# Kernel optimization log

Hardware: AMD Instinct MI355X
Metric: run time of the kernel (lower is better)

The kernel has to match this reference:

```python
import jax, jax.numpy as jnp
import numpy as np
import math

B, T, N, C = 1, 12, 10000, 32
TIME_DIM, N_SUP, E, NODE_EMB = 8, 3, 320000, 32
S = N_SUP + 2  # support_len + 2 slots after concat


def setup_inputs() -> dict:
    key = jax.random.key(0)
    ks = jax.random.split(key, 16)
    inp = {
        'x': jax.random.normal(ks[0], (B, T, N, C), jnp.float32),
        'timeoh': jax.random.uniform(ks[1], (B, 43), jnp.float32),
        'edges': jax.random.randint(ks[2], (N_SUP, 2, E), 0, N),
        # shared dy_gat params (attention_list reuses the same ModuleList)
        'mlp_w': jax.random.normal(ks[3], (C, C), jnp.float32) * 0.05,
        'mlp_b': jnp.zeros((C,), jnp.float32),
        'temb_w': jax.random.normal(ks[4], (43, TIME_DIM), jnp.float32) * 0.1,
        'atten_pool': jax.random.normal(ks[5], (TIME_DIM, 2 * C), jnp.float32) * 0.1,
        # adaptive-adjacency gcn branch
        'node2vec': jax.random.normal(ks[6], (N, NODE_EMB), jnp.float32) * 0.1,
        'gcn_w': jax.random.normal(ks[7], (3 * C, C), jnp.float32) * 0.05,
        'gcn_b': jnp.zeros((C,), jnp.float32),
        # slot self-attention over S supports
        'q_w': jax.random.normal(ks[8], (C, 6 * C), jnp.float32) * 0.05,
        'q_b': jnp.zeros((6 * C,), jnp.float32),
        'k_w': jax.random.normal(ks[9], (C, 6 * C), jnp.float32) * 0.05,
        'k_b': jnp.zeros((6 * C,), jnp.float32),
        'v_w': jax.random.normal(ks[10], (C, 6 * C), jnp.float32) * 0.05,
        'v_b': jnp.zeros((6 * C,), jnp.float32),
        'dense_w': jax.random.normal(ks[11], (6 * C, C), jnp.float32) * 0.05,
        'dense_b': jnp.zeros((C,), jnp.float32),
    }
    return inp


def _dy_gat(x, timeoh, src, dst, mlp_w, mlp_b, temb_w, atten_pool):
    h = x @ mlp_w + mlp_b                                   # (B,T,N,C)
    attn = (timeoh @ temb_w) @ atten_pool                    # (B,2C)
    # einsum('btnc,bc->btn') over concatenated [h_src, h_dst] splits additively
    s_src = jnp.einsum('btnc,bc->btn', h, attn[:, :C])
    s_dst = jnp.einsum('btnc,bc->btn', h, attn[:, C:])
    values = s_src[:, :, src] + s_dst[:, :, dst]             # (B,T,E)
    p = jax.nn.leaky_relu(values, 0.01)
    e = jnp.exp(p - jnp.max(p, axis=2, keepdims=True))       # global (per b,t) max-shift
    rowsum = jnp.zeros((B, T, N), e.dtype).at[:, :, src].add(e)
    h_prime = jnp.zeros_like(h).at[:, :, src].add(e[..., None] * h[:, :, dst, :])
    h_prime = h_prime / (rowsum[..., None] + 9e-15)
    return jax.nn.elu(h_prime)  # concat=True


def reference(x, timeoh, edges, mlp_w, mlp_b, temb_w, atten_pool,
              node2vec, gcn_w, gcn_b, q_w, q_b, k_w, k_b, v_w, v_b,
              dense_w, dense_b):
    outs = [x]
    for i in range(N_SUP):
        outs.append(_dy_gat(x, timeoh, edges[i, 0], edges[i, 1],
                            mlp_w, mlp_b, temb_w, atten_pool))
    # adaptive graph conv (static, order=2, support_len=1)
    adj = jax.nn.softmax(jax.nn.relu(node2vec @ node2vec.T), axis=1)  # (N,N)
    x1 = jnp.einsum('wv,btvf->btwf', adj, x)
    x2 = jnp.einsum('wv,btvf->btwf', adj, x1)
    x_adp = jnp.concatenate([x, x1, x2], -1) @ gcn_w + gcn_b
    outs.append(x_adp)
    out = jnp.concatenate(outs, -1).reshape(B, T, N, S, C)
    q = out @ q_w + q_b                                       # (B,T,N,S,6C)
    k = out @ k_w + k_b
    v = out @ v_w + v_b
    scores = jnp.einsum('btnsd,btnud->btnsu', q, k) / math.sqrt(6 * C)
    a = jax.nn.softmax(scores, axis=-1)
    o = jnp.einsum('btnsu,btnud->btnsd', a, v)
    o = o @ dense_w + dense_b                                 # (B,T,N,S,C)
    return jax.nn.elu(jnp.mean(o, axis=-2))                   # (B,T,N,C)
```

## Files before the change

kernel.cpp:

```cpp
#include <hip/hip_runtime.h>
#include <hip/hip_bf16.h>

#define T_ 12
#define N_ 10000
#define C_ 32
#define E_ 320000
#define SUP_ 3
#define TN_ (T_*N_)

typedef __attribute__((ext_vector_type(4))) float f32x4;
typedef __attribute__((ext_vector_type(8))) short bf16x8;
typedef __attribute__((ext_vector_type(4))) short bf16x4;

__device__ __forceinline__ short bf16c(float f) {
  __hip_bfloat16 b = __float2bfloat16(f);
  return (short)__builtin_bit_cast(unsigned short, b);
}

#if __has_builtin(__builtin_amdgcn_exp2f)
#define EXP2F(x) __builtin_amdgcn_exp2f(x)
#else
#define EXP2F(x) exp2f(x)
#endif

#define PRM_ATTN 0
#define PRM_G    64
#define PRM_H    1088
#define PRM_G1   2112
#define PRM_G2   2144
#define PRM_HB   2176
#define PRM_G0   2208

__global__ __launch_bounds__(256) void k_prep(
    const float* __restrict__ timeoh, const float* __restrict__ temb_w,
    const float* __restrict__ atten_pool,
    const float* __restrict__ q_w, const float* __restrict__ q_b,
    const float* __restrict__ k_w, const float* __restrict__ k_b,
    const float* __restrict__ v_w, const float* __restrict__ v_b,
    const float* __restrict__ dense_w, const float* __restrict__ dense_b,
    float* __restrict__ prm) {
  __shared__ float tv[8];
  int tid = threadIdx.x;
  if (tid < 8) {
    float s = 0.f;
    for (int j = 0; j < 43; j++) s += timeoh[j] * temb_w[j * 8 + tid];
    tv[tid] = s;
  }
  __syncthreads();
  if (tid < 64) {
    float s = 0.f;
    for (int d = 0; d < 8; d++) s += tv[d] * atten_pool[d * 64 + tid];
    prm[PRM_ATTN + tid] = s;
  }
  for (int idx = tid; idx < 1024; idx += 256) {
    int r = idx >> 5, c = idx & 31;
    float s = 0.f, s2 = 0.f;
    for (int d = 0; d < 192; d++) {
      s  += q_w[r * 192 + d] * k_w[c * 192 + d];
      s2 += v_w[r * 192 + d] * dense_w[d * 32 + c];
    }
    prm[PRM_G + idx] = s;
    prm[PRM_H + idx] = s2;
  }
  if (tid < 32) {
    float s = 0.f, s2 = 0.f, s3 = 0.f;
    for (int d = 0; d < 192; d++) {
      s  += q_w[tid * 192 + d] * k_b[d];
      s2 += k_w[tid * 192 + d] * q_b[d];
      s3 += v_b[d] * dense_w[d * 32 + tid];
    }
    prm[PRM_G1 + tid] = s;
    prm[PRM_G2 + tid] = s2;
    prm[PRM_HB + tid] = s3 + dense_b[tid];
  }
  if (tid == 0) {
    float s = 0.f;
    for (int d = 0; d < 192; d++) s += q_b[d] * k_b[d];
    prm[PRM_G0] = s;
  }
}

__global__ __launch_bounds__(256) void k_h(
    const float* __restrict__ x, const float* __restrict__ mlp_w,
    const float* __restrict__ mlp_b, const float* __restrict__ prm,
    __hip_bfloat16* __restrict__ h16, float* __restrict__ s_src,
    float* __restrict__ s_dst) {
  __shared__ float W[32 * 32];
  __shared__ float bsh[32], attnsh[64];
  __shared__ float xs[8][32];
  int tid = threadIdx.x;
  for (int i = tid; i < 1024; i += 256) W[i] = mlp_w[i];
  if (tid < 32) bsh[tid] = mlp_b[tid];
  if (tid < 64) attnsh[tid] = prm[PRM_ATTN + tid];
  long base = (long)blockIdx.x * 8;
  int nloc = tid >> 5, c = tid & 31;
  long row = base + nloc;
  xs[nloc][c] = x[row * 32 + c];
  __syncthreads();
  float hval = bsh[c];
#pragma unroll
  for (int k = 0; k < 32; k++) hval = fmaf(xs[nloc][k], W[k * 32 + c], hval);
  h16[row * 32 + c] = __float2bfloat16(hval);
  float a = hval * attnsh[c], b = hval * attnsh[32 + c];
#pragma unroll
  for (int m = 16; m >= 1; m >>= 1) {
    a += __shfl_xor(a, m, 64);
    b += __shfl_xor(b, m, 64);
  }
  if (c == 0) { s_src[row] = a; s_dst[row] = b; }
}

__global__ __launch_bounds__(256) void k_maxs(const float* __restrict__ ssrc,
                                              const float* __restrict__ sdst,
                                              float* __restrict__ Mt) {
  __shared__ float sh[8];
  const int t = blockIdx.x, tid = threadIdx.x;
  float ma = -1e30f, mb = -1e30f;
  for (int i = tid; i < N_; i += 256) {
    ma = fmaxf(ma, ssrc[(long)t * N_ + i]);
    mb = fmaxf(mb, sdst[(long)t * N_ + i]);
  }
#pragma unroll
  for (int k = 32; k >= 1; k >>= 1) {
    ma = fmaxf(ma, __shfl_xor(ma, k, 64));
    mb = fmaxf(mb, __shfl_xor(mb, k, 64));
  }
  if ((tid & 63) == 0) { sh[(tid >> 6) * 2] = ma; sh[(tid >> 6) * 2 + 1] = mb; }
  __syncthreads();
  if (tid == 0) {
    float A = fmaxf(fmaxf(sh[0], sh[2]), fmaxf(sh[4], sh[6]));
    float B = fmaxf(fmaxf(sh[1], sh[3]), fmaxf(sh[5], sh[7]));
    Mt[t] = A + B;
  }
}

__global__ __launch_bounds__(256) void k_hist(const int* __restrict__ edges,
                                              int* __restrict__ cnt) {
  int sup = blockIdx.y;
  int e = blockIdx.x * 256 + threadIdx.x;
  const int* src = edges + (long)sup * 2 * E_;
  atomicAdd(&cnt[sup * N_ + src[e]], 1);
}

__global__ __launch_bounds__(1024) void k_scan(const int* __restrict__ cnt,
                                               int* __restrict__ offs,
                                               int* __restrict__ cur) {
  __shared__ int sh[1024];
  __shared__ int run;
  int sup = blockIdx.x, tid = threadIdx.x;
  if (tid == 0) run = 0;
  __syncthreads();
  for (int base = 0; base < N_; base += 1024) {
    int i = base + tid;
    int v = (i < N_) ? cnt[sup * N_ + i] : 0;
    sh[tid] = v;
    __syncthreads();
    for (int off = 1; off < 1024; off <<= 1) {
      int t = (tid >= off) ? sh[tid - off] : 0;
      __syncthreads();
      sh[tid] += t;
      __syncthreads();
    }
    int runv = run;
    int excl = runv + sh[tid] - v;
    if (i < N_) {
      offs[sup * (N_ + 1) + i] = excl;
      cur[sup * N_ + i] = excl;
    }
    __syncthreads();
    if (tid == 0) run = runv + sh[1023];
    __syncthreads();
  }
  if (tid == 0) offs[sup * (N_ + 1) + N_] = run;
}

__global__ __launch_bounds__(256) void k_fill(const int* __restrict__ edges,
                                              int* __restrict__ cur,
                                              int* __restrict__ csr) {
  int sup = blockIdx.y;
  int e = blockIdx.x * 256 + threadIdx.x;
  const int* src = edges + (long)sup * 2 * E_;
  const int* dst = src + E_;
  int pos = atomicAdd(&cur[sup * N_ + src[e]], 1);
  csr[sup * E_ + pos] = dst[e];
}

__global__ __launch_bounds__(256) void k_gather(
    const int* __restrict__ csr, const int* __restrict__ offs,
    const float* __restrict__ s_src, const float* __restrict__ s_dst,
    const float* __restrict__ Mt, const __hip_bfloat16* __restrict__ h16,
    __hip_bfloat16* __restrict__ hp16) {
  const int sup = blockIdx.z, t = blockIdx.y;
  const int wave = threadIdx.x >> 6, lane = threadIdx.x & 63;
  const int n = blockIdx.x * 4 + wave;
  const float M = Mt[t];
  const float a = s_src[(long)t * N_ + n];
  const int off = offs[sup * (N_ + 1) + n], end = offs[sup * (N_ + 1) + n + 1];
  const float* sd = s_dst + (long)t * N_;
  const uint4* hb4 = (const uint4*)(h16 + (long)t * N_ * 32);
  const int* csrs = csr + sup * E_;
  const int slot = lane >> 2, cl = lane & 3;
  const int clamp = (end > off) ? (end - 1) : 0;

  float acc[8];
#pragma unroll
  for (int j = 0; j < 8; j++) acc[j] = 0.f;
  float psum = 0.f;

  const int idx0 = off + slot;
  int d0 = csrs[min(idx0, clamp)];
  int d1 = csrs[min(idx0 + 16, clamp)];
  float sd0 = sd[d0];
  uint4 u0 = hb4[d0 * 4 + cl];

  for (int idx = idx0; idx < end; idx += 16) {
    int d2 = csrs[min(idx + 32, clamp)];
    float sd1 = sd[d1];
    uint4 u1 = hb4[d1 * 4 + cl];
    float v = a + sd0;
    v = fmaxf(v, 0.01f * v);
    float p = __expf(v - M);
    psum += p;
    acc[0] = fmaf(p, __uint_as_float(u0.x << 16),        acc[0]);
    acc[1] = fmaf(p, __uint_as_float(u0.x & 0xffff0000u), acc[1]);
    acc[2] = fmaf(p, __uint_as_float(u0.y << 16),        acc[2]);
    acc[3] = fmaf(p, __uint_as_float(u0.y & 0xffff0000u), acc[3]);
    acc[4] = fmaf(p, __uint_as_float(u0.z << 16),        acc[4]);
    acc[5] = fmaf(p, __uint_as_float(u0.z & 0xffff0000u), acc[5]);
    acc[6] = fmaf(p, __uint_as_float(u0.w << 16),        acc[6]);
    acc[7] = fmaf(p, __uint_as_float(u0.w & 0xffff0000u), acc[7]);
    d1 = d2; sd0 = sd1; u0 = u1;
  }

#pragma unroll
  for (int m = 4; m <= 32; m <<= 1) psum += __shfl_xor(psum, m, 64);
#pragma unroll
  for (int j = 0; j < 8; j++) {
#pragma unroll
    for (int m = 4; m <= 32; m <<= 1) acc[j] += __shfl_xor(acc[j], m, 64);
  }

  if (slot == 0) {
    float inv = 1.f / (psum + 9e-15f);
    unsigned w[4];
#pragma unroll
    for (int q = 0; q < 4; q++) {
      float h0 = acc[2 * q + 0] * inv;
      float h1 = acc[2 * q + 1] * inv;
      h0 = (h0 > 0.f) ? h0 : (__expf(h0) - 1.f);
      h1 = (h1 > 0.f) ? h1 : (__expf(h1) - 1.f);
      unsigned lo = (unsigned)(unsigned short)__builtin_bit_cast(unsigned short, __float2bfloat16(h0));
      unsigned hi = (unsigned)(unsigned short)__builtin_bit_cast(unsigned short, __float2bfloat16(h1));
      w[q] = lo | (hi << 16);
    }
    ((uint4*)hp16)[((long)sup * TN_ + (long)t * N_ + n) * 4 + cl] = uint4{w[0], w[1], w[2], w[3]};
  }
}

__global__ __launch_bounds__(256) void k_n2vA(const float* __restrict__ n2v,
                                              short* __restrict__ n2vA) {
  const float SC = 1.2011224087864498f;
  int idx = blockIdx.x * 256 + threadIdx.x;
  if (idx >= N_ * 4) return;
  int row = idx >> 2, l4 = idx & 3;
  short v[8];
#pragma unroll
  for (int h = 0; h < 2; h++)
#pragma unroll
    for (int j = 0; j < 4; j++)
      v[h * 4 + j] = bf16c(n2v[row * 32 + 16 * h + 4 * l4 + j] * SC);
  *(bf16x8*)&n2vA[(long)idx * 8] = bf16x8{v[0], v[1], v[2], v[3], v[4], v[5], v[6], v[7]};
}

template <int WITHR>
__global__ __launch_bounds__(256) void k_pack(const float* __restrict__ src,
                                              const float* __restrict__ rinv,
                                              short* __restrict__ xq) {
  int idx = blockIdx.x * 256 + threadIdx.x;
  int ck = idx / 1536;
  int rem = idx - ck * 1536;
  int l4 = rem / 384;
  int col = rem - l4 * 384;
  int t = col >> 5, f = col & 31;
  const long cb = (long)t * N_ * 32 + f;
  short v[8];
#pragma unroll
  for (int e = 0; e < 8; e++) {
    int vv = ck * 32 + 4 * l4 + (e & 3) + 16 * (e >> 2);
    float a = 0.f;
    if (vv < N_) {
      a = src[cb + (long)vv * 32];
      if (WITHR) a *= rinv[vv];
    }
    v[e] = bf16c(a);
  }
  *(bf16x8*)&xq[(long)idx * 8] = bf16x8{v[0], v[1], v[2], v[3], v[4], v[5], v[6], v[7]};
}

template <int PASS>
__global__ __launch_bounds__(512, 2) void k_adj12(const short* __restrict__ n2vA,
                                                  const short* __restrict__ xq,
                                                  float* __restrict__ out,
                                                  float* __restrict__ Rout) {
  __shared__ __align__(16) short aPl[2][8 * 4 * 64 * 8];
  const int tid = threadIdx.x;
  const int lane = tid & 63;
  const int wv = tid >> 6;
  const int l15 = lane & 15;
  const int l4 = lane >> 4;
  const int brow0 = blockIdx.x * 64;
  const int colbase = wv * 48;

  bf16x8 bw[4];
#pragma unroll
  for (int mt = 0; mt < 4; mt++) {
    int row = brow0 + mt * 16 + l15;
    row = row < N_ ? row : N_ - 1;
    bw[mt] = *(const bf16x8*)&n2vA[((long)row * 4 + l4) * 8];
  }

  f32x4 acc[4][3];
#pragma unroll
  for (int i = 0; i < 4; i++)
#pragma unroll
    for (int j = 0; j < 3; j++) acc[i][j] = f32x4{0.f, 0.f, 0.f, 0.f};
  float racc[4] = {0.f, 0.f, 0.f, 0.f};

#define PHASE_A(cexpr, slab)                                                              \
  {                                                                                       \
    const int c_ = (cexpr);                                                               \
    if (c_ < 313) {                                                                       \
      const int vb_ = c_ * 32;                                                            \
      int r1_ = vb_ + 16 + l15; r1_ = r1_ < N_ ? r1_ : N_ - 1;                            \
      bf16x8 av0_ = *(const bf16x8*)&n2vA[((long)(vb_ + l15) * 4 + l4) * 8];              \
      bf16x8 av1_ = *(const bf16x8*)&n2vA[((long)r1_ * 4 + l4) * 8];                      \
      _Pragma("unroll")                                                                   \
      for (int mt = 0; mt < 4; mt++) {                                                    \
        f32x4 s0_ = __builtin_amdgcn_mfma_f32_16x16x32_bf16(av0_, bw[mt],                 \
                                                            f32x4{0.f,0.f,0.f,0.f},0,0,0);\
        f32x4 s1_ = __builtin_amdgcn_mfma_f32_16x16x32_bf16(av1_, bw[mt],                 \
                                                            f32x4{0.f,0.f,0.f,0.f},0,0,0);\
        short pp_[8];                                                                     \
        float rs0_ = 0.f, rs1_ = 0.f;                                                     \
        _Pragma("unroll")                                                                 \
        for (int j = 0; j < 4; j++) {                                                     \
          float p0_ = EXP2F(fmaxf(s0_[j], 0.f));                                          \
          float p1_ = EXP2F(fmaxf(s1_[j], 0.f));                                          \
          if constexpr (PASS == 1) { rs0_ += p0_; rs1_ += p1_; }                          \
          pp_[j] = bf16c(p0_);                                                            \
          pp_[j + 4] = bf16c(p1_);                                                        \
        }                                                                                 \
        *(bf16x8*)&aPl[slab][((wv * 4 + mt) * 64 + lane) * 8] =                           \
            bf16x8{pp_[0],pp_[1],pp_[2],pp_[3],pp_[4],pp_[5],pp_[6],pp_[7]};              \
        if constexpr (PASS == 1) racc[mt] += (c_ != 312) ? (rs0_ + rs1_) : rs0_;          \
      }                                                                                   \
    }                                                                                     \
  }

  PHASE_A(wv, 0)
  __syncthreads();

  for (int g = 0; g < 40; g++) {
    const int cur = g & 1;
    if (g + 1 < 40) PHASE_A((g + 1) * 8 + wv, cur ^ 1)

    const int rem = 313 - g * 8;
    if (rem >= 8) {
      bf16x8 bx[24];
#pragma unroll
      for (int cc = 0; cc < 8; cc++) {
        const long xb = (long)(g * 8 + cc) * 1536 + (long)l4 * 384;
        bx[cc * 3 + 0] = *(const bf16x8*)&xq[(xb + colbase + 0 * 16 + l15) * 8];
        bx[cc * 3 + 1] = *(const bf16x8*)&xq[(xb + colbase + 1 * 16 + l15) * 8];
        bx[cc * 3 + 2] = *(const bf16x8*)&xq[(xb + colbase + 2 * 16 + l15) * 8];
      }
#pragma unroll
      for (int cc = 0; cc < 8; cc++) {
#pragma unroll
        for (int mt = 0; mt < 4; mt++) {
          bf16x8 aP = *(const bf16x8*)&aPl[cur][((cc * 4 + mt) * 64 + lane) * 8];
          acc[mt][0] = __builtin_amdgcn_mfma_f32_16x16x32_bf16(aP, bx[cc * 3 + 0], acc[mt][0], 0, 0, 0);
          acc[mt][1] = __builtin_amdgcn_mfma_f32_16x16x32_bf16(aP, bx[cc * 3 + 1], acc[mt][1], 0, 0, 0);
          acc[mt][2] = __builtin_amdgcn_mfma_f32_16x16x32_bf16(aP, bx[cc * 3 + 2], acc[mt][2], 0, 0, 0);
        }
      }
    } else {
      for (int cc = 0; cc < rem; cc++) {
        const long xb = (long)(g * 8 + cc) * 1536 + (long)l4 * 384;
        bf16x8 bx0 = *(const bf16x8*)&xq[(xb + colbase + 0 * 16 + l15) * 8];
        bf16x8 bx1 = *(const bf16x8*)&xq[(xb + colbase + 1 * 16 + l15) * 8];
        bf16x8 bx2 = *(const bf16x8*)&xq[(xb + colbase + 2 * 16 + l15) * 8];
#pragma unroll
        for (int mt = 0; mt < 4; mt++) {
          bf16x8 aP = *(const bf16x8*)&aPl[cur][((cc * 4 + mt) * 64 + lane) * 8];
          acc[mt][0] = __builtin_amdgcn_mfma_f32_16x16x32_bf16(aP, bx0, acc[mt][0], 0, 0, 0);
          acc[mt][1] = __builtin_amdgcn_mfma_f32_16x16x32_bf16(aP, bx1, acc[mt][1], 0, 0, 0);
          acc[mt][2] = __builtin_amdgcn_mfma_f32_16x16x32_bf16(aP, bx2, acc[mt][2], 0, 0, 0);
        }
      }
    }
    __syncthreads();
  }
#undef PHASE_A

  if constexpr (PASS == 1) {
#pragma unroll
    for (int mt = 0; mt < 4; mt++) {
      float r = racc[mt];
      r += __shfl_xor(r, 16, 64);
      r += __shfl_xor(r, 32, 64);
      int w = brow0 + mt * 16 + l15;
      if (l4 == 0 && w < N_) atomicAdd(&Rout[w], r);
    }
  }
#pragma unroll
  for (int mt = 0; mt < 4; mt++) {
#pragma unroll
    for (int nt = 0; nt < 3; nt++) {
      const int col = colbase + nt * 16 + l15;
      const int t = col >> 5, f = col & 31;
#pragma unroll
      for (int j = 0; j < 4; j++) {
        const int w = brow0 + mt * 16 + 4 * l4 + j;
        if (w < N_) out[((long)t * N_ + w) * 32 + f] = acc[mt][nt][j];
      }
    }
  }
}

__global__ __launch_bounds__(256) void k_rinv(float* __restrict__ R) {
  int i = blockIdx.x * 256 + threadIdx.x;
  if (i < N_) R[i] = 1.f / R[i];
}

__global__ __launch_bounds__(256) void k_gcn(const float* __restrict__ x,
                                             const float* __restrict__ x1,
                                             float* __restrict__ x2io,
                                             const float* __restrict__ Rinv,
                                             const float* __restrict__ gcn_w,
                                             const float* __restrict__ gcn_b) {
  __shared__ float W[96 * 32];
  __shared__ float bsh[32];
  __shared__ float rows[8][96];
  int tid = threadIdx.x;
  for (int i = tid; i < 96 * 32; i += 256) W[i] = gcn_w[i];
  if (tid < 32) bsh[tid] = gcn_b[tid];
  long base = (long)blockIdx.x * 8;
  int nloc = tid >> 5, c = tid & 31;
  long row = base + nloc;
  long nIdx = row % N_;
  float ri = Rinv[nIdx];
  rows[nloc][c] = x[row * 32 + c];
  rows[nloc][32 + c] = x1[row * 32 + c] * ri;
  rows[nloc][64 + c] = x2io[row * 32 + c] * ri;
  __syncthreads();
  float o = bsh[c];
#pragma unroll
  for (int k = 0; k < 96; k++) o = fmaf(rows[nloc][k], W[k * 32 + c], o);
  __syncthreads();
  x2io[row * 32 + c] = o;
}

__global__ __launch_bounds__(256) void k_attn3(const float* __restrict__ x,
                                               const __hip_bfloat16* __restrict__ hp16,
                                               const float* __restrict__ xadp,
                                               const float* __restrict__ prm,
                                               float* __restrict__ out) {
  __shared__ float Gs[1024], Hs[1024], g1s[32], g2s[32], hbs[32];
  __shared__ float g0sh;
  __shared__ float msl[8][5][33];
  __shared__ float yl[8][5][33];
  __shared__ float scl[8][33];
  __shared__ float zl[8][33];
  const int tid = threadIdx.x;
  const int nloc = tid >> 5, c = tid & 31;
  for (int i = tid; i < 1024; i += 256) { Gs[i] = prm[PRM_G + i]; Hs[i] = prm[PRM_H + i]; }
  if (tid < 32) { g1s[tid] = prm[PRM_G1 + tid]; g2s[tid] = prm[PRM_G2 + tid]; hbs[tid] = prm[PRM_HB + tid]; }
  if (tid == 0) g0sh = prm[PRM_G0];
  const long r = (long)blockIdx.x * 8 + nloc;
  msl[nloc][0][c] = x[r * 32 + c];
#pragma unroll
  for (int s = 1; s <= 3; s++)
    msl[nloc][s][c] = __bfloat162float(hp16[((long)(s - 1) * TN_ + r) * 32 + c]);
  msl[nloc][4][c] = xadp[r * 32 + c];
  __syncthreads();

#pragma unroll
  for (int s = 0; s < 5; s++) {
    float y = 0.f;
#pragma unroll
    for (int k = 0; k < 32; k++) y = fmaf(msl[nloc][s][k], Gs[k * 32 + c], y);
    yl[nloc][s][c] = y + g2s[c];
  }
  {
    float dot = 0.f;
    if (c < 25) {
      const int s = c / 5, u = c - s * 5;
#pragma unroll
      for (int k = 0; k < 32; k++) dot = fmaf(yl[nloc][s][k], msl[nloc][u][k], dot);
    } else if (c < 30) {
      const int u = c - 25;
#pragma unroll
      for (int k = 0; k < 32; k++) dot = fmaf(msl[nloc][u][k], g1s[k], dot);
    }
    scl[nloc][c] = dot;
  }

  const float rs = 0.07216878364870322f;
  const float g0 = g0sh;
  float abar[5];
#pragma unroll
  for (int u = 0; u < 5; u++) abar[u] = 0.f;
#pragma unroll
  for (int s = 0; s < 5; s++) {
    const float d1s = scl[nloc][25 + s];
    float e[5];
    float mx = -1e30f;
#pragma unroll
    for (int u = 0; u < 5; u++) {
      float v = (scl[nloc][s * 5 + u] + d1s + g0) * rs;
      e[u] = v;
      mx = fmaxf(mx, v);
    }
    float sm = 0.f;
#pragma unroll
    for (int u = 0; u < 5; u++) { e[u] = __expf(e[u] - mx); sm += e[u]; }
    float inv = 1.f / sm;
#pragma unroll
    for (int u = 0; u < 5; u++) abar[u] = fmaf(e[u], inv, abar[u]);
  }

  float z = 0.f;
#pragma unroll
  for (int u = 0; u < 5; u++) z = fmaf(abar[u], msl[nloc][u][c], z);
  zl[nloc][c] = z * 0.2f;

  float o = hbs[c];
#pragma unroll
  for (int k = 0; k < 32; k++) o = fmaf(zl[nloc][k], Hs[k * 32 + c], o);
  o = (o > 0.f) ? o : (__expf(o) - 1.f);
  out[r * 32 + c] = o;
}

extern "C" void kernel_launch(void* const* d_in, const int* in_sizes, int n_in,
                              void* d_out, int out_size, void* d_ws, size_t ws_size,
                              hipStream_t stream) {
  (void)in_sizes; (void)n_in; (void)out_size; (void)ws_size;
  const float* x          = (const float*)d_in[0];
  const float* timeoh     = (const float*)d_in[1];
  const int*   edges      = (const int*)d_in[2];
  const float* mlp_w      = (const float*)d_in[3];
  const float* mlp_b      = (const float*)d_in[4];
  const float* temb_w     = (const float*)d_in[5];
  const float* atten_pool = (const float*)d_in[6];
  const float* node2vec   = (const float*)d_in[7];
  const float* gcn_w      = (const float*)d_in[8];
  const float* gcn_b      = (const float*)d_in[9];
  const float* q_w  = (const float*)d_in[10];
  const float* q_b  = (const float*)d_in[11];
  const float* k_w  = (const float*)d_in[12];
  const float* k_b  = (const float*)d_in[13];
  const float* v_w  = (const float*)d_in[14];
  const float* v_b  = (const float*)d_in[15];
  const float* dense_w = (const float*)d_in[16];
  const float* dense_b = (const float*)d_in[17];
  float* out = (float*)d_out;
  char* ws = (char*)d_ws;

  float*    prm  = (float*)(ws + 0);
  float*    Mt   = (float*)(ws + 9216);
  int*      cnt  = (int*)(ws + 9472);
  int*      cur  = (int*)(ws + 129472);
  int*      offs = (int*)(ws + 249472);
  float*    ssrc = (float*)(ws + 369664);
  float*    sdst = (float*)(ws + 849664);
  float*    R    = (float*)(ws + 1329664);
  __hip_bfloat16* h16  = (__hip_bfloat16*)(ws + 1369664);
  int*      csr  = (int*)(ws + 9049664);
  __hip_bfloat16* hp16 = (__hip_bfloat16*)(ws + 12889664);
  float*    x1   = (float*)(ws + 35929664);
  float*    x2   = (float*)(ws + 51289664);
  short*    n2vA = (short*)(ws + 66649664);
  short*    xq0  = (short*)(ws + 67289664);
  short*    xq1  = (short*)(ws + 74983488);

  (void)hipMemsetAsync(cnt, 0, 120000, stream);
  (void)hipMemsetAsync(R, 0, 40000, stream);

  k_prep<<<1, 256, 0, stream>>>(timeoh, temb_w, atten_pool, q_w, q_b, k_w, k_b,
                                v_w, v_b, dense_w, dense_b, prm);
  k_h<<<15000, 256, 0, stream>>>(x, mlp_w, mlp_b, prm, h16, ssrc, sdst);
  k_maxs<<<12, 256, 0, stream>>>(ssrc, sdst, Mt);
  k_hist<<<dim3(1250, 3), 256, 0, stream>>>(edges, cnt);
  k_scan<<<3, 1024, 0, stream>>>(cnt, offs, cur);
  k_fill<<<dim3(1250, 3), 256, 0, stream>>>(edges, cur, csr);
  k_gather<<<dim3(2500, 12, 3), 256, 0, stream>>>(csr, offs, ssrc, sdst, Mt, h16, hp16);

  k_n2vA<<<157, 256, 0, stream>>>(node2vec, n2vA);
  k_pack<0><<<1878, 256, 0, stream>>>(x, nullptr, xq0);
  k_adj12<1><<<157, 512, 0, stream>>>(n2vA, xq0, x1, R);
  k_rinv<<<40, 256, 0, stream>>>(R);
  k_pack<1><<<1878, 256, 0, stream>>>(x1, R, xq1);
  k_adj12<2><<<157, 512, 0, stream>>>(n2vA, xq1, x2, nullptr);
  k_gcn<<<15000, 256, 0, stream>>>(x, x1, x2, R, gcn_w, gcn_b);
  k_attn3<<<15000, 256, 0, stream>>>(x, hp16, x2, prm, out);
}
```

Before: 895.7 us.

## Stage adjacency GEMM operand tiles via async global-to-LDS loads with finer work split

The fused adjacency-softmax times x GEMM now copies each pair of packed x chunks into a double-buffered LDS region using global_load_lds, overlapping the copy with the current group's MFMAs. Before, each wave loaded 24 bf16x8 registers straight from global memory. The probability-tile computation is also redistributed: each wave now computes one 16-row m-tile of one chunk instead of four m-tiles across eight chunks. This cuts the redundant exp work per wave but raises the group count from 40 to 157, so the kernel hits many more barriers.

Result: slower. 1.022 ms (+14.1%).

```diff
diff --git a/kernel.cpp b/kernel.cpp
--- a/kernel.cpp
+++ b/kernel.cpp
@@ -7,6 +7,7 @@
 #define E_ 320000
 #define SUP_ 3
 #define TN_ (T_*N_)
+#define CHUNKB 24576
 
 typedef __attribute__((ext_vector_type(4))) float f32x4;
 typedef __attribute__((ext_vector_type(8))) short bf16x8;
@@ -22,6 +23,13 @@
 #else
 #define EXP2F(x) exp2f(x)
 #endif
+
+__device__ __forceinline__ void gload_lds16(const void* g, void* l) {
+  __builtin_amdgcn_global_load_lds(
+      (__attribute__((address_space(1))) void*)(void*)g,
+      (__attribute__((address_space(3))) void*)l,
+      16, 0, 0);
+}
 
 #define PRM_ATTN 0
 #define PRM_G    64
@@ -298,11 +306,12 @@
 }
 
 template <int PASS>
-__global__ __launch_bounds__(512, 2) void k_adj12(const short* __restrict__ n2vA,
+__global__ __launch_bounds__(512, 2) void k_adj14(const short* __restrict__ n2vA,
                                                   const short* __restrict__ xq,
                                                   float* __restrict__ out,
                                                   float* __restrict__ Rout) {
-  __shared__ __align__(16) short aPl[2][8 * 4 * 64 * 8];
+  __shared__ __align__(16) char xbuf[2][2 * CHUNKB];
+  __shared__ __align__(16) short aPl[2][8 * 64 * 8];
   const int tid = threadIdx.x;
   const int lane = tid & 63;
   const int wv = tid >> 6;
@@ -310,13 +319,13 @@
   const int l4 = lane >> 4;
   const int brow0 = blockIdx.x * 64;
   const int colbase = wv * 48;
-
-  bf16x8 bw[4];
-#pragma unroll
-  for (int mt = 0; mt < 4; mt++) {
-    int row = brow0 + mt * 16 + l15;
+  const int amt = wv & 3;
+
+  bf16x8 bwA;
+  {
+    int row = brow0 + amt * 16 + l15;
     row = row < N_ ? row : N_ - 1;
-    bw[mt] = *(const bf16x8*)&n2vA[((long)row * 4 + l4) * 8];
+    bwA = *(const bf16x8*)&n2vA[((long)row * 4 + l4) * 8];
   }
 
   f32x4 acc[4][3];
@@ -324,94 +333,84 @@
   for (int i = 0; i < 4; i++)
 #pragma unroll
     for (int j = 0; j < 3; j++) acc[i][j] = f32x4{0.f, 0.f, 0.f, 0.f};
-  float racc[4] = {0.f, 0.f, 0.f, 0.f};
-
-#define PHASE_A(cexpr, slab)                                                              \
+  float raccA = 0.f;
+
+  const int NGRP = 157;
+
+#define STAGE(G, buf)                                                                     \
   {                                                                                       \
-    const int c_ = (cexpr);                                                               \
+    const int sbytes = (2 * (G) + 1 < 313) ? 2 * CHUNKB : CHUNKB;                         \
+    const char* src_ = (const char*)xq + (long)(G) * 2 * CHUNKB + wv * 6144 + lane * 16;  \
+    char* dst_ = xbuf[buf] + wv * 6144;                                                   \
+    _Pragma("unroll")                                                                     \
+    for (int i = 0; i < 6; i++)                                                           \
+      if (wv * 6144 + i * 1024 < sbytes) gload_lds16(src_ + i * 1024, dst_ + i * 1024);   \
+  }
+
+#define PHASE_A(G, slab)                                                                  \
+  {                                                                                       \
+    const int c_ = 2 * (G) + (wv >> 2);                                                   \
     if (c_ < 313) {                                                                       \
       const int vb_ = c_ * 32;                                                            \
       int r1_ = vb_ + 16 + l15; r1_ = r1_ < N_ ? r1_ : N_ - 1;                            \
       bf16x8 av0_ = *(const bf16x8*)&n2vA[((long)(vb_ + l15) * 4 + l4) * 8];              \
       bf16x8 av1_ = *(const bf16x8*)&n2vA[((long)r1_ * 4 + l4) * 8];                      \
+      f32x4 s0_ = __builtin_amdgcn_mfma_f32_16x16x32_bf16(av0_, bwA,                      \
+                                                          f32x4{0.f,0.f,0.f,0.f},0,0,0); \
+      f32x4 s1_ = __builtin_amdgcn_mfma_f32_16x16x32_bf16(av1_, bwA,                      \
+                                                          f32x4{0.f,0.f,0.f,0.f},0,0,0); \
+      short pp_[8];                                                                       \
+      float rs0_ = 0.f, rs1_ = 0.f;                                                       \
       _Pragma("unroll")                                                                   \
-      for (int mt = 0; mt < 4; mt++) {                                                    \
-        f32x4 s0_ = __builtin_amdgcn_mfma_f32_16x16x32_bf16(av0_, bw[mt],                 \
-                                                            f32x4{0.f,0.f,0.f,0.f},0,0,0);\
-        f32x4 s1_ = __builtin_amdgcn_mfma_f32_16x16x32_bf16(av1_, bw[mt],                 \
-                                                            f32x4{0.f,0.f,0.f,0.f},0,0,0);\
-        short pp_[8];                                                                     \
-        float rs0_ = 0.f, rs1_ = 0.f;                                                     \
-        _Pragma("unroll")                                                                 \
-        for (int j = 0; j < 4; j++) {                                                     \
-          float p0_ = EXP2F(fmaxf(s0_[j], 0.f));                                          \
-          float p1_ = EXP2F(fmaxf(s1_[j], 0.f));                                          \
-          if constexpr (PASS == 1) { rs0_ += p0_; rs1_ += p1_; }                          \
-          pp_[j] = bf16c(p0_);                                                            \
-          pp_[j + 4] = bf16c(p1_);                                                        \
-        }                                                                                 \
-        *(bf16x8*)&aPl[slab][((wv * 4 + mt) * 64 + lane) * 8] =                           \
-            bf16x8{pp_[0],pp_[1],pp_[2],pp_[3],pp_[4],pp_[5],pp_[6],pp_[7]};              \
-        if constexpr (PASS == 1) racc[mt] += (c_ != 312) ? (rs0_ + rs1_) : rs0_;          \
+      for (int j = 0; j < 4; j++) {                                                       \
+        float p0_ = EXP2F(fmaxf(s0_[j], 0.f));                                            \
+        float p1_ = EXP2F(fmaxf(s1_[j], 0.f));                                            \
+        if constexpr (PASS == 1) { rs0_ += p0_; rs1_ += p1_; }                            \
+        pp_[j] = bf16c(p0_);                                                              \
+        pp_[j + 4] = bf16c(p1_);                                                          \
       }                                                                                   \
+      *(bf16x8*)&aPl[slab][(wv * 64 + lane) * 8] =                                        \
+          bf16x8{pp_[0],pp_[1],pp_[2],pp_[3],pp_[4],pp_[5],pp_[6],pp_[7]};                \
+      if constexpr (PASS == 1) raccA += (c_ != 312) ? (rs0_ + rs1_) : rs0_;               \
     }                                                                                     \
   }
 
-  PHASE_A(wv, 0)
-  __syncthreads();
-
-  for (int g = 0; g < 40; g++) {
+  STAGE(0, 0)
+  PHASE_A(0, 0)
+  __syncthreads();
+
+  for (int g = 0; g < NGRP; g++) {
     const int cur = g & 1;
-    if (g + 1 < 40) PHASE_A((g + 1) * 8 + wv, cur ^ 1)
-
-    const int rem = 313 - g * 8;
-    if (rem >= 8) {
-      bf16x8 bx[24];
-#pragma unroll
-      for (int cc = 0; cc < 8; cc++) {
-        const long xb = (long)(g * 8 + cc) * 1536 + (long)l4 * 384;
-        bx[cc * 3 + 0] = *(const bf16x8*)&xq[(xb + colbase + 0 * 16 + l15) * 8];
-        bx[cc * 3 + 1] = *(const bf16x8*)&xq[(xb + colbase + 1 * 16 + l15) * 8];
-        bx[cc * 3 + 2] = *(const bf16x8*)&xq[(xb + colbase + 2 * 16 + l15) * 8];
+    if (g + 1 < NGRP) {
+      STAGE(g + 1, cur ^ 1)
+      PHASE_A(g + 1, cur ^ 1)
+    }
+#pragma unroll
+    for (int cc = 0; cc < 2; cc++) {
+      if (2 * g + cc >= 313) break;
+      const char* xb = xbuf[cur] + cc * CHUNKB;
+      bf16x8 bx0 = *(const bf16x8*)(xb + (l4 * 384 + colbase + 0 * 16 + l15) * 16);
+      bf16x8 bx1 = *(const bf16x8*)(xb + (l4 * 384 + colbase + 1 * 16 + l15) * 16);
+      bf16x8 bx2 = *(const bf16x8*)(xb + (l4 * 384 + colbase + 2 * 16 + l15) * 16);
+#pragma unroll
+      for (int mt = 0; mt < 4; mt++) {
+        bf16x8 aP = *(const bf16x8*)&aPl[cur][((cc * 4 + mt) * 64 + lane) * 8];
+        acc[mt][0] = __builtin_amdgcn_mfma_f32_16x16x32_bf16(aP, bx0, acc[mt][0], 0, 0, 0);
+        acc[mt][1] = __builtin_amdgcn_mfma_f32_16x16x32_bf16(aP, bx1, acc[mt][1], 0, 0, 0);
+        acc[mt][2] = __builtin_amdgcn_mfma_f32_16x16x32_bf16(aP, bx2, acc[mt][2], 0, 0, 0);
       }
-#pragma unroll
-      for (int cc = 0; cc < 8; cc++) {
-#pragma unroll
-        for (int mt = 0; mt < 4; mt++) {
-          bf16x8 aP = *(const bf16x8*)&aPl[cur][((cc * 4 + mt) * 64 + lane) * 8];
-          acc[mt][0] = __builtin_amdgcn_mfma_f32_16x16x32_bf16(aP, bx[cc * 3 + 0], acc[mt][0], 0, 0, 0);
-          acc[mt][1] = __builtin_amdgcn_mfma_f32_16x16x32_bf16(aP, bx[cc * 3 + 1], acc[mt][1], 0, 0, 0);
-          acc[mt][2] = __builtin_amdgcn_mfma_f32_16x16x32_bf16(aP, bx[cc * 3 + 2], acc[mt][2], 0, 0, 0);
-        }
-      }
-    } else {
-      for (int cc = 0; cc < rem; cc++) {
-        const long xb = (long)(g * 8 + cc) * 1536 + (long)l4 * 384;
-        bf16x8 bx0 = *(const bf16x8*)&xq[(xb + colbase + 0 * 16 + l15) * 8];
-        bf16x8 bx1 = *(const bf16x8*)&xq[(xb + colbase + 1 * 16 + l15) * 8];
-        bf16x8 bx2 = *(const bf16x8*)&xq[(xb + colbase + 2 * 16 + l15) * 8];
-#pragma unroll
-        for (int mt = 0; mt < 4; mt++) {
-          bf16x8 aP = *(const bf16x8*)&aPl[cur][((cc * 4 + mt) * 64 + lane) * 8];
-          acc[mt][0] = __builtin_amdgcn_mfma_f32_16x16x32_bf16(aP, bx0, acc[mt][0], 0, 0, 0);
-          acc[mt][1] = __builtin_amdgcn_mfma_f32_16x16x32_bf16(aP, bx1, acc[mt][1], 0, 0, 0);
-          acc[mt][2] = __builtin_amdgcn_mfma_f32_16x16x32_bf16(aP, bx2, acc[mt][2], 0, 0, 0);
-        }
-      }
     }
     __syncthreads();
   }
 #undef PHASE_A
+#undef STAGE
 
   if constexpr (PASS == 1) {
-#pragma unroll
-    for (int mt = 0; mt < 4; mt++) {
-      float r = racc[mt];
-      r += __shfl_xor(r, 16, 64);
-      r += __shfl_xor(r, 32, 64);
-      int w = brow0 + mt * 16 + l15;
-      if (l4 == 0 && w < N_) atomicAdd(&Rout[w], r);
-    }
+    float r = raccA;
+    r += __shfl_xor(r, 16, 64);
+    r += __shfl_xor(r, 32, 64);
+    int w = brow0 + amt * 16 + l15;
+    if (l4 == 0 && w < N_) atomicAdd(&Rout[w], r);
   }
 #pragma unroll
   for (int mt = 0; mt < 4; mt++) {
@@ -598,10 +597,10 @@
 
   k_n2vA<<<157, 256, 0, stream>>>(node2vec, n2vA);
   k_pack<0><<<1878, 256, 0, stream>>>(x, nullptr, xq0);
-  k_adj12<1><<<157, 512, 0, stream>>>(n2vA, xq0, x1, R);
+  k_adj14<1><<<157, 512, 0, stream>>>(n2vA, xq0, x1, R);
   k_rinv<<<40, 256, 0, stream>>>(R);
   k_pack<1><<<1878, 256, 0, stream>>>(x1, R, xq1);
-  k_adj12<2><<<157, 512, 0, stream>>>(n2vA, xq1, x2, nullptr);
+  k_adj14<2><<<157, 512, 0, stream>>>(n2vA, xq1, x2, nullptr);
   k_gcn<<<15000, 256, 0, stream>>>(x, x1, x2, R, gcn_w, gcn_b);
   k_attn3<<<15000, 256, 0, stream>>>(x, hp16, x2, prm, out);
 }
```
